# Performance work log

Measured on AMD Instinct MI355X. Metric: run time of the kernel, lower is better.

The kernel has to match this reference:

```python
import jax, jax.numpy as jnp
import numpy as np

EMB = 1024
HEADS = 16
DK = EMB // HEADS

def setup_inputs() -> dict:
    key = jax.random.key(0)
    ks = jax.random.split(key, 5)
    scale = 0.02
    return {
        "x": jax.random.normal(ks[0], (4, 2048, EMB), dtype=jnp.float32),
        "W_in": jax.random.normal(ks[1], (3 * EMB, EMB), dtype=jnp.float32) * scale,
        "b_in": jax.random.normal(ks[2], (3 * EMB,), dtype=jnp.float32) * scale,
        "W_out": jax.random.normal(ks[3], (EMB, EMB), dtype=jnp.float32) * scale,
        "b_out": jax.random.normal(ks[4], (EMB,), dtype=jnp.float32) * scale,
    }

def reference(x, W_in, b_in, W_out, b_out):
    B, T, C = x.shape
    qkv = x @ W_in.T + b_in                      # [B,T,3C]
    q, k, v = jnp.split(qkv, 3, axis=-1)
    def heads(t):
        return t.reshape(B, T, HEADS, DK).transpose(0, 2, 1, 3)  # [B,H,T,Dk]
    q, k, v = heads(q), heads(k), heads(v)
    scores = jnp.einsum("bhqd,bhkd->bhqk", q, k) / jnp.sqrt(jnp.float32(DK))
    causal = jnp.tril(jnp.ones((T, T), dtype=bool))
    scores = jnp.where(causal, scores, jnp.finfo(scores.dtype).min)
    attn = jax.nn.softmax(scores, axis=-1)
    y = jnp.einsum("bhqk,bhkd->bhqd", attn, v)   # [B,H,T,Dk]
    y = y.transpose(0, 2, 1, 3).reshape(B, T, C)
    return y @ W_out.T + b_out
```

## Files before the change

### kernel.cpp

```cpp
#include <hip/hip_runtime.h>
#include <hip/hip_bf16.h>

#define EMB   1024
#define HEADS 16
#define DKV   64
#define BB    4
#define TT    2048
#define MTOT  8192

#define QSCALE 0.1803368801111204f

typedef short bf16x8 __attribute__((ext_vector_type(8)));
typedef float f32x4  __attribute__((ext_vector_type(4)));

__device__ __forceinline__ ushort bf16_bits(float f) {
    union { __hip_bfloat16 h; ushort u; } cv;
    cv.h = __float2bfloat16(f);
    return cv.u;
}
__device__ __forceinline__ unsigned pack_bf16(float lo, float hi) {
    return (unsigned)bf16_bits(lo) | ((unsigned)bf16_bits(hi) << 16);
}
__device__ __forceinline__ void gload16(const void* g, void* lds) {
    __builtin_amdgcn_global_load_lds(
        (const __attribute__((address_space(1))) unsigned*)g,
        (__attribute__((address_space(3))) unsigned*)lds, 16, 0, 0);
}
__device__ __forceinline__ int swz128(int row, int bytecol) {
    return row * 128 + (bytecol ^ ((row & 7) << 4));
}

__global__ void cvt_all(const float* __restrict__ x,   ushort* __restrict__ xo,
                        const float* __restrict__ wi,  ushort* __restrict__ wio,
                        const float* __restrict__ wo,  ushort* __restrict__ woo) {
    const int n4x = (MTOT * EMB) / 4;
    const int n4i = (3 * EMB * EMB) / 4;
    const int n4o = (EMB * EMB) / 4;
    int idx = blockIdx.x * blockDim.x + threadIdx.x;
    int stride = gridDim.x * blockDim.x;
    for (int i = idx; i < n4x + n4i + n4o; i += stride) {
        const float* in;
        ushort* out;
        int j = i;
        if (j < n4x)            { in = x;  out = xo;  }
        else if (j < n4x + n4i) { in = wi; out = wio; j -= n4x; }
        else                    { in = wo; out = woo; j -= n4x + n4i; }
        float4 v = reinterpret_cast<const float4*>(in)[j];
        ushort4 o;
        o.x = bf16_bits(v.x);
        o.y = bf16_bits(v.y);
        o.z = bf16_bits(v.z);
        o.w = bf16_bits(v.w);
        reinterpret_cast<ushort4*>(out)[j] = o;
    }
}

template<int EPI>
__global__ __launch_bounds__(256) void gemm_bt(
    const ushort* __restrict__ Ab, const ushort* __restrict__ Wb,
    const float* __restrict__ bias,
    ushort* __restrict__ qo, ushort* __restrict__ ko, ushort* __restrict__ vo,
    float* __restrict__ outf,
    int Msz, int Nsz, int Ksz)
{
    __shared__ __align__(16) ushort Sh[6][128 * 32];

    int tid = threadIdx.x;
    int mtiles = Msz >> 7;
    int bm = blockIdx.x % mtiles;
    int bn = blockIdx.x / mtiles;
    int m0 = bm << 7, n0 = bn << 7;
    int w = tid >> 6, l = tid & 63;
    int wr = w >> 1, wc = w & 1;
    int lr = l & 15, lk = (l >> 4) << 3;
    int srow = w * 16 + (l >> 2);
    int scol = (l & 3) << 3;

    f32x4 acc[4][4] = {};

    auto STAGE = [&](int buf, int k0) {
        #pragma unroll
        for (int p = 0; p < 2; ++p) {
            int row = p * 64 + srow;
            gload16(&Ab[(size_t)(m0 + row) * Ksz + k0 + scol],
                    (char*)Sh[buf * 2]     + (size_t)(p * 256 + w * 64) * 16);
            gload16(&Wb[(size_t)(n0 + row) * Ksz + k0 + scol],
                    (char*)Sh[buf * 2 + 1] + (size_t)(p * 256 + w * 64) * 16);
        }
    };

    const int nk = Ksz >> 5;
    STAGE(0, 0);
    STAGE(1, 32);
    int buf = 0, sbuf = 2;
    for (int t = 0; t < nk; ++t) {
        if (t + 1 < nk) asm volatile("s_waitcnt vmcnt(4)" ::: "memory");
        else            asm volatile("s_waitcnt vmcnt(0)" ::: "memory");
        __builtin_amdgcn_s_barrier();
        __builtin_amdgcn_sched_barrier(0);

        const ushort* As = Sh[buf * 2];
        const ushort* Bs = Sh[buf * 2 + 1];
        bf16x8 a[4], b[4];
        #pragma unroll
        for (int mi = 0; mi < 4; ++mi)
            a[mi] = *(const bf16x8*)(&As[(wr * 64 + mi * 16 + lr) * 32 + lk]);
        #pragma unroll
        for (int ni = 0; ni < 4; ++ni)
            b[ni] = *(const bf16x8*)(&Bs[(wc * 64 + ni * 16 + lr) * 32 + lk]);

        if (t + 2 < nk) STAGE(sbuf, (t + 2) << 5);

        __builtin_amdgcn_s_setprio(1);
        #pragma unroll
        for (int mi = 0; mi < 4; ++mi)
            #pragma unroll
            for (int ni = 0; ni < 4; ++ni)
                acc[mi][ni] = __builtin_amdgcn_mfma_f32_16x16x32_bf16(
                    a[mi], b[ni], acc[mi][ni], 0, 0, 0);
        __builtin_amdgcn_s_setprio(0);

        buf = (buf == 2) ? 0 : buf + 1;
        sbuf = (sbuf == 2) ? 0 : sbuf + 1;
    }

    if (EPI == 1) {
        #pragma unroll
        for (int mi = 0; mi < 4; ++mi)
            #pragma unroll
            for (int ni = 0; ni < 4; ++ni) {
                int n = n0 + wc * 64 + ni * 16 + lr;
                float bv = bias[n];
                #pragma unroll
                for (int r = 0; r < 4; ++r) {
                    int m = m0 + wr * 64 + mi * 16 + ((l >> 4) << 2) + r;
                    outf[(size_t)m * Nsz + n] = acc[mi][ni][r] + bv;
                }
            }
    } else {
        int which = n0 >> 10;
        if (which < 2) {
            ushort* dst = (which == 0) ? qo : ko;
            float qs = (which == 0) ? QSCALE : 1.f;
            #pragma unroll
            for (int mi = 0; mi < 4; ++mi)
                #pragma unroll
                for (int ni = 0; ni < 4; ++ni) {
                    int n = n0 + wc * 64 + ni * 16 + lr;
                    float bv = bias[n];
                    int rem = n & 1023;
                    int hd = rem >> 6, dk = rem & 63;
                    #pragma unroll
                    for (int r = 0; r < 4; ++r) {
                        int m = m0 + wr * 64 + mi * 16 + ((l >> 4) << 2) + r;
                        int b_ = m >> 11, t_ = m & 2047;
                        dst[((((size_t)b_ * HEADS + hd) * TT + t_) << 6) + dk] =
                            bf16_bits((acc[mi][ni][r] + bv) * qs);
                    }
                }
        } else {
            char* Tb = (char*)Sh;
            int b_ = m0 >> 11;
            int row_r = tid >> 1;
            int rem = (n0 + row_r) & 1023;
            int hd = rem >> 6, dk = rem & 63;
            size_t vrow = ((size_t)(b_ * HEADS + hd) * DKV + dk) * TT;
            int tbase = (m0 & 2047) + (tid & 1) * 32;
            #pragma unroll
            for (int h = 0; h < 2; ++h) {
                __syncthreads();
                if (wr == h) {
                    #pragma unroll
                    for (int ni = 0; ni < 4; ++ni) {
                        int n_l = wc * 64 + ni * 16 + lr;
                        float bv = bias[n0 + n_l];
                        #pragma unroll
                        for (int mi = 0; mi < 4; ++mi) {
                            uint2 u;
                            u.x = pack_bf16(acc[mi][ni][0] + bv, acc[mi][ni][1] + bv);
                            u.y = pack_bf16(acc[mi][ni][2] + bv, acc[mi][ni][3] + bv);
                            *(uint2*)(Tb + swz128(n_l, mi * 32 + ((l >> 4) << 3))) = u;
                        }
                    }
                }
                __syncthreads();
                #pragma unroll
                for (int qq = 0; qq < 4; ++qq) {
                    int4 d = *(const int4*)(Tb + swz128(row_r, (tid & 1) * 64 + qq * 16));
                    *(int4*)(&vo[vrow + tbase + h * 64 + qq * 8]) = d;
                }
            }
        }
    }
}

__device__ __forceinline__ void strip_tile(
    const char* __restrict__ Kbuf, const char* __restrict__ Vbuf, char* __restrict__ Plw,
    bf16x8 q0, bf16x8 q1,
    float& l_run, f32x4 (&o)[4],
    int lr, int g, bool diag, int qloc)
{
    f32x4 st[4];
    #pragma unroll
    for (int kt = 0; kt < 4; ++kt) {
        bf16x8 a0 = *(const bf16x8*)(Kbuf + swz128(kt * 16 + lr, g * 16));
        bf16x8 a1 = *(const bf16x8*)(Kbuf + swz128(kt * 16 + lr, 64 + g * 16));
        f32x4 z = {};
        __builtin_amdgcn_s_setprio(1);
        z = __builtin_amdgcn_mfma_f32_16x16x32_bf16(a0, q0, z, 0, 0, 0);
        z = __builtin_amdgcn_mfma_f32_16x16x32_bf16(a1, q1, z, 0, 0, 0);
        __builtin_amdgcn_s_setprio(0);
        st[kt] = z;
    }
    if (diag) {
        #pragma unroll
        for (int kt = 0; kt < 4; ++kt)
            #pragma unroll
            for (int r = 0; r < 4; ++r) {
                int kvloc = kt * 16 + g * 4 + r;
                st[kt][r] = (kvloc <= qloc) ? st[kt][r] : -1e30f;
            }
    }

    float rs = 0.f;
    #pragma unroll
    for (int kt = 0; kt < 4; ++kt) {
        float p0 = exp2f(st[kt][0]);
        float p1 = exp2f(st[kt][1]);
        float p2 = exp2f(st[kt][2]);
        float p3 = exp2f(st[kt][3]);
        rs += (p0 + p1) + (p2 + p3);
        uint2 u;
        u.x = pack_bf16(p0, p1);
        u.y = pack_bf16(p2, p3);
        *(uint2*)(Plw + swz128(lr, kt * 32 + g * 8)) = u;
    }
    l_run += rs;

    bf16x8 pa0 = *(const bf16x8*)(Plw + swz128(lr, g * 16));
    bf16x8 pa1 = *(const bf16x8*)(Plw + swz128(lr, 64 + g * 16));

    __builtin_amdgcn_s_setprio(1);
    #pragma unroll
    for (int dt = 0; dt < 4; ++dt) {
        bf16x8 b0 = *(const bf16x8*)(Vbuf + swz128(dt * 16 + lr, g * 16));
        bf16x8 b1 = *(const bf16x8*)(Vbuf + swz128(dt * 16 + lr, 64 + g * 16));
        o[dt] = __builtin_amdgcn_mfma_f32_16x16x32_bf16(pa0, b0, o[dt], 0, 0, 0);
        o[dt] = __builtin_amdgcn_mfma_f32_16x16x32_bf16(pa1, b1, o[dt], 0, 0, 0);
    }
    __builtin_amdgcn_s_setprio(0);
}

__global__ __launch_bounds__(256, 3) void attn_kernel(
    const ushort* __restrict__ qb, const ushort* __restrict__ kb,
    const ushort* __restrict__ vtb, ushort* __restrict__ yb)
{
    __shared__ __align__(16) char Ks[2][64 * 128];
    __shared__ __align__(16) char Vs[2][64 * 128];
    __shared__ __align__(16) char Pl[4][16 * 128];

    int tid = threadIdx.x;
    int w = tid >> 6, l = tid & 63;
    int bid = blockIdx.x;
    int swz = (bid & 7) * 128 + (bid >> 3);
    int pair = swz & 15;
    int bh = swz >> 4;
    int qtA = 31 - pair, qtB = pair;

    const ushort* Q  = qb  + (size_t)bh * TT * DKV;
    const ushort* K  = kb  + (size_t)bh * TT * DKV;
    const ushort* Vt = vtb + (size_t)bh * DKV * TT;
    int lr = l & 15, g = l >> 4;
    int qA0 = qtA * 64 + w * 16;
    int qB0 = qtB * 64 + w * 16;

    bf16x8 qaA0 = *(const bf16x8*)(&Q[(size_t)(qA0 + lr) * DKV + g * 8]);
    bf16x8 qaA1 = *(const bf16x8*)(&Q[(size_t)(qA0 + lr) * DKV + 32 + g * 8]);
    bf16x8 qaB0 = *(const bf16x8*)(&Q[(size_t)(qB0 + lr) * DKV + g * 8]);
    bf16x8 qaB1 = *(const bf16x8*)(&Q[(size_t)(qB0 + lr) * DKV + 32 + g * 8]);

    int srow = w * 8 + (l >> 3);
    int scel = ((((l & 7) * 16) ^ ((l >> 3) << 4)) >> 1);

    float lA = 0.f, lB = 0.f;
    f32x4 oA[4] = {}, oB[4] = {};
    int nt = qtA + 1;

    #pragma unroll
    for (int p = 0; p < 2; ++p) {
        int row = p * 32 + srow;
        gload16(&K [(size_t)row * DKV + scel], (char*)Ks[0] + (size_t)(p * 256 + w * 64) * 16);
        gload16(&Vt[(size_t)row * TT  + scel], (char*)Vs[0] + (size_t)(p * 256 + w * 64) * 16);
    }

    for (int jt = 0; jt < nt; ++jt) {
        int buf = jt & 1;
        __syncthreads();

        if (jt + 1 < nt) {
            int kv1 = (jt + 1) * 64;
            #pragma unroll
            for (int p = 0; p < 2; ++p) {
                int row = p * 32 + srow;
                gload16(&K [(size_t)(kv1 + row) * DKV + scel],
                        (char*)Ks[buf ^ 1] + (size_t)(p * 256 + w * 64) * 16);
                gload16(&Vt[(size_t)row * TT + kv1 + scel],
                        (char*)Vs[buf ^ 1] + (size_t)(p * 256 + w * 64) * 16);
            }
        }

        strip_tile(Ks[buf], Vs[buf], Pl[w], qaA0, qaA1, lA, oA,
                   lr, g, jt == qtA, w * 16 + lr);
        if (jt <= qtB)
            strip_tile(Ks[buf], Vs[buf], Pl[w], qaB0, qaB1, lB, oB,
                       lr, g, jt == qtB, w * 16 + lr);
    }

    lA += __shfl_xor(lA, 16);
    lA += __shfl_xor(lA, 32);
    lB += __shfl_xor(lB, 16);
    lB += __shfl_xor(lB, 32);

    int b_ = bh >> 4, h_ = bh & 15;
    {
        float li0 = 1.f / __shfl(lA, g * 4 + 0);
        float li1 = 1.f / __shfl(lA, g * 4 + 1);
        float li2 = 1.f / __shfl(lA, g * 4 + 2);
        float li3 = 1.f / __shfl(lA, g * 4 + 3);
        #pragma unroll
        for (int dt = 0; dt < 4; ++dt) {
            int d_ = h_ * 64 + dt * 16 + lr;
            size_t base = ((size_t)b_ * TT + (qA0 + g * 4)) * EMB + d_;
            yb[base]           = bf16_bits(oA[dt][0] * li0);
            yb[base + EMB]     = bf16_bits(oA[dt][1] * li1);
            yb[base + 2 * EMB] = bf16_bits(oA[dt][2] * li2);
            yb[base + 3 * EMB] = bf16_bits(oA[dt][3] * li3);
        }
    }
    {
        float li0 = 1.f / __shfl(lB, g * 4 + 0);
        float li1 = 1.f / __shfl(lB, g * 4 + 1);
        float li2 = 1.f / __shfl(lB, g * 4 + 2);
        float li3 = 1.f / __shfl(lB, g * 4 + 3);
        #pragma unroll
        for (int dt = 0; dt < 4; ++dt) {
            int d_ = h_ * 64 + dt * 16 + lr;
            size_t base = ((size_t)b_ * TT + (qB0 + g * 4)) * EMB + d_;
            yb[base]           = bf16_bits(oB[dt][0] * li0);
            yb[base + EMB]     = bf16_bits(oB[dt][1] * li1);
            yb[base + 2 * EMB] = bf16_bits(oB[dt][2] * li2);
            yb[base + 3 * EMB] = bf16_bits(oB[dt][3] * li3);
        }
    }
}

extern "C" void kernel_launch(void* const* d_in, const int* in_sizes, int n_in,
                              void* d_out, int out_size, void* d_ws, size_t ws_size,
                              hipStream_t stream) {
    const float* x     = (const float*)d_in[0];
    const float* W_in  = (const float*)d_in[1];
    const float* b_in  = (const float*)d_in[2];
    const float* W_out = (const float*)d_in[3];
    const float* b_out = (const float*)d_in[4];
    float* out = (float*)d_out;
    char* ws = (char*)d_ws;

    ushort* xb  = (ushort*)(ws);
    ushort* wib = (ushort*)(ws + 16777216);
    ushort* wob = (ushort*)(ws + 23068672);
    ushort* qbp = (ushort*)(ws + 25165824);
    ushort* kbp = (ushort*)(ws + 41943040);
    ushort* vbp = (ushort*)(ws + 58720256);
    ushort* ybp = (ushort*)(ws + 75497472);

    cvt_all<<<1280, 256, 0, stream>>>(x, xb, W_in, wib, W_out, wob);

    gemm_bt<0><<<dim3((MTOT / 128) * (3 * EMB / 128)), dim3(256), 0, stream>>>(
        xb, wib, b_in, qbp, kbp, vbp, nullptr, MTOT, 3 * EMB, EMB);

    attn_kernel<<<dim3(BB * HEADS * 16), dim3(256), 0, stream>>>(
        qbp, kbp, vbp, ybp);

    gemm_bt<1><<<dim3((MTOT / 128) * (EMB / 128)), dim3(256), 0, stream>>>(
        ybp, wob, b_out, nullptr, nullptr, nullptr, out, MTOT, EMB, EMB);
}
```

Before: 172.3 us.

## Redistribute softmax probabilities via cross-lane shuffles instead of LDS round trip

The P tile from the QK^T MFMA output is no longer written to per-wave LDS and read back in A-operand layout. It is repacked in registers with two xor-shuffles per packed word and lane-dependent selects. The P buffer is removed from shared memory, which shrinks LDS use, and launch bounds rise from 3 to 4 blocks per SM. The cost is extra shuffle and select instructions and tighter register limits at the higher occupancy target, which could cause spills.

```diff
diff --git a/kernel.cpp b/kernel.cpp
--- a/kernel.cpp
+++ b/kernel.cpp
@@ -195,10 +195,11 @@
 }
 
 __device__ __forceinline__ void strip_tile(
-    const char* __restrict__ Kbuf, const char* __restrict__ Vbuf, char* __restrict__ Plw,
+    const char* __restrict__ Kbuf, const char* __restrict__ Vbuf,
     bf16x8 q0, bf16x8 q1,
     float& l_run, f32x4 (&o)[4],
-    int lr, int g, bool diag, int qloc)
+    int lr, int g, bool diag, int qloc,
+    bool lowhalf, bool g0, bool g1, bool g2, bool g3, bool geven)
 {
     f32x4 st[4];
     #pragma unroll
@@ -223,22 +224,46 @@
     }
 
     float rs = 0.f;
+    float pv[4][4];
     #pragma unroll
-    for (int kt = 0; kt < 4; ++kt) {
-        float p0 = exp2f(st[kt][0]);
-        float p1 = exp2f(st[kt][1]);
-        float p2 = exp2f(st[kt][2]);
-        float p3 = exp2f(st[kt][3]);
-        rs += (p0 + p1) + (p2 + p3);
-        uint2 u;
-        u.x = pack_bf16(p0, p1);
-        u.y = pack_bf16(p2, p3);
-        *(uint2*)(Plw + swz128(lr, kt * 32 + g * 8)) = u;
-    }
+    for (int kt = 0; kt < 4; ++kt)
+        #pragma unroll
+        for (int r = 0; r < 4; ++r) {
+            pv[kt][r] = exp2f(st[kt][r]);
+            rs += pv[kt][r];
+        }
     l_run += rs;
 
-    bf16x8 pa0 = *(const bf16x8*)(Plw + swz128(lr, g * 16));
-    bf16x8 pa1 = *(const bf16x8*)(Plw + swz128(lr, 64 + g * 16));
+    unsigned Aq[4], Bq[4];
+    Aq[0] = pack_bf16(pv[0][0], pv[0][1]);
+    Aq[1] = pack_bf16(pv[0][2], pv[0][3]);
+    Aq[2] = pack_bf16(pv[2][0], pv[2][1]);
+    Aq[3] = pack_bf16(pv[2][2], pv[2][3]);
+    Bq[0] = pack_bf16(pv[1][0], pv[1][1]);
+    Bq[1] = pack_bf16(pv[1][2], pv[1][3]);
+    Bq[2] = pack_bf16(pv[3][0], pv[3][1]);
+    Bq[3] = pack_bf16(pv[3][2], pv[3][3]);
+
+    unsigned p0w[4], p1w[4];
+    #pragma unroll
+    for (int j = 0; j < 4; ++j) {
+        unsigned M = lowhalf ? Bq[j] : Aq[j];
+        unsigned Msw = (unsigned)__shfl_xor((int)M, 32);
+        unsigned S = g0 ? Aq[j] : (g3 ? Bq[j] : Msw);
+        unsigned E = g1 ? Aq[j] : (g2 ? Bq[j] : Msw);
+        unsigned Sx = (unsigned)__shfl_xor((int)E, 16);
+        unsigned F = geven ? S : Sx;
+        unsigned G = geven ? Sx : S;
+        if (j == 0)      { p0w[0] = F; p0w[2] = G; }
+        else if (j == 1) { p0w[1] = F; p0w[3] = G; }
+        else if (j == 2) { p1w[0] = F; p1w[2] = G; }
+        else             { p1w[1] = F; p1w[3] = G; }
+    }
+    int4 t0, t1;
+    t0.x = p0w[0]; t0.y = p0w[1]; t0.z = p0w[2]; t0.w = p0w[3];
+    t1.x = p1w[0]; t1.y = p1w[1]; t1.z = p1w[2]; t1.w = p1w[3];
+    bf16x8 pa0 = *(bf16x8*)&t0;
+    bf16x8 pa1 = *(bf16x8*)&t1;
 
     __builtin_amdgcn_s_setprio(1);
     #pragma unroll
@@ -251,13 +276,12 @@
     __builtin_amdgcn_s_setprio(0);
 }
 
-__global__ __launch_bounds__(256, 3) void attn_kernel(
+__global__ __launch_bounds__(256, 4) void attn_kernel(
     const ushort* __restrict__ qb, const ushort* __restrict__ kb,
     const ushort* __restrict__ vtb, ushort* __restrict__ yb)
 {
     __shared__ __align__(16) char Ks[2][64 * 128];
     __shared__ __align__(16) char Vs[2][64 * 128];
-    __shared__ __align__(16) char Pl[4][16 * 128];
 
     int tid = threadIdx.x;
     int w = tid >> 6, l = tid & 63;
@@ -271,6 +295,9 @@
     const ushort* K  = kb  + (size_t)bh * TT * DKV;
     const ushort* Vt = vtb + (size_t)bh * DKV * TT;
     int lr = l & 15, g = l >> 4;
+    bool lowhalf = (l < 32);
+    bool g0 = (g == 0), g1 = (g == 1), g2 = (g == 2), g3 = (g == 3);
+    bool geven = ((g & 1) == 0);
     int qA0 = qtA * 64 + w * 16;
     int qB0 = qtB * 64 + w * 16;
 
@@ -309,11 +336,11 @@
             }
         }
 
-        strip_tile(Ks[buf], Vs[buf], Pl[w], qaA0, qaA1, lA, oA,
-                   lr, g, jt == qtA, w * 16 + lr);
+        strip_tile(Ks[buf], Vs[buf], qaA0, qaA1, lA, oA,
+                   lr, g, jt == qtA, w * 16 + lr, lowhalf, g0, g1, g2, g3, geven);
         if (jt <= qtB)
-            strip_tile(Ks[buf], Vs[buf], Pl[w], qaB0, qaB1, lB, oB,
-                       lr, g, jt == qtB, w * 16 + lr);
+            strip_tile(Ks[buf], Vs[buf], qaB0, qaB1, lB, oB,
+                       lr, g, jt == qtB, w * 16 + lr, lowhalf, g0, g1, g2, g3, geven);
     }
 
     lA += __shfl_xor(lA, 16);
```

After: 180.6 us. 1.05x slower.
